# Kernel optimization log

Measured on AMD Instinct MI355X. Metric: run time of the kernel, lower is better.

The kernel has to match this reference:

```python
import jax, jax.numpy as jnp
import numpy as np
from jax import lax

# flat indices of the 8 'donut' taps in a 3x3 kernel (center position 4 stays zero),
# matching torch.nonzero row-major ordering of the mask
_DONUT_IDX = jnp.array([0, 1, 2, 3, 5, 6, 7, 8])

def _gelu(x):
    return jax.nn.gelu(x, approximate=False)  # torch nn.GELU default (erf)

def _conv(x, w, dil=1, pad=0):
    return lax.conv_general_dilated(x, w, (1, 1), [(pad, pad), (pad, pad)],
                                    rhs_dilation=(dil, dil),
                                    dimension_numbers=('NCHW', 'OIHW', 'NCHW'))

def _donut_conv(x, p, dil):
    # ParamConv_reg_variable_dilation with shuffle_true=0: scatter 8 params into a
    # 3x3 kernel (zero center) and conv with rhs_dilation=dil, padding=dil ('same').
    O, I, _ = p.shape
    k = jnp.zeros((O, I, 9), p.dtype).at[:, :, _DONUT_IDX].set(p).reshape(O, I, 3, 3)
    return _conv(x, k, dil=dil, pad=dil)

def _resblock(x, w1, w2):
    # gelu(Sequential(conv3x3, gelu, conv3x3)(x) + x)
    return _gelu(_conv(_gelu(_conv(x, w1, pad=1)), w2, pad=1) + x)

def _avgpool2(x):
    N, C, H, W = x.shape
    return x.reshape(N, C, H // 2, 2, W // 2, 2).mean(axis=(3, 5))

def _upsample(x, scale, w):
    # nn.Upsample(scale, bilinear, align_corners=False) -> half-pixel bilinear resize
    N, C, H, W = x.shape
    if scale > 1:
        x = jax.image.resize(x, (N, C, H * scale, W * scale), method='bilinear')
    return _gelu(_conv(x, w))  # 1x1 conv + gelu

def _shine_fwd(input_image, conv0a_w, conv0b_w, first_p, cl10_w, cl2_w,
               dil_p, dilres_p, ups_w, out1_w, out2_w, last_w):
    # n_frames=5, center frame index 2; H,W divisible by 64 so no pad branch
    target = input_image[:, 2:3]
    feats = jnp.concatenate([input_image[:, :2], input_image[:, 3:]], axis=1)  # [N,4,H,W]
    target = _gelu(_conv(target, conv0b_w))            # 1x1 -> 48 ch
    feats = _gelu(_conv(feats, conv0a_w, pad=1))       # 3x3 -> 16 ch
    base = jnp.concatenate([target, feats], axis=1)    # 64 ch

    outs = [_gelu(_donut_conv(base, first_p, 1))]      # first_output (dil 1)
    base = _resblock(base, cl10_w[0, 0], cl10_w[0, 1])
    outs.append(_gelu(_donut_conv(base, dilres_p[0], 3)))  # dilated_convs_res[0]
    base = _resblock(base, cl2_w[0, 0], cl2_w[0, 1])

    dils = (5, 8, 10, 11)     # dilated_convs effective dilations (add_dilation=0)
    dilres = (3, 6, 8, 9)     # dilated_convs_res effective dilations
    for i in range(4):
        m = _gelu(_donut_conv(base, dil_p[i], dils[i]))
        outs.append(_upsample(m, 2 ** i, ups_w[i]))
        if i < 3:
            base = _avgpool2(base)
            base = _resblock(base, cl10_w[i + 1, 0], cl10_w[i + 1, 1])
            m = _gelu(_donut_conv(base, dilres_p[i + 1], dilres[i + 1]))
            outs.append(_upsample(m, 2 ** (i + 1), ups_w[i + 1]))
            base = _resblock(base, cl2_w[i + 1, 0], cl2_w[i + 1, 1])

    out = jnp.concatenate(outs, axis=1)                # 9*64 = 576 ch
    out = _gelu(_conv(out, out1_w))                    # 1x1 576->288
    out = _gelu(_conv(out, out2_w))                    # 1x1 288->64
    return _conv(out, last_w)                          # 1x1 64->1

def setup_inputs():
    key = jax.random.key(0)
    ks = jax.random.split(key, 12)
    s = 0.05
    F = 64
    return {
        'input_image': jax.random.normal(ks[0], (2, 5, 256, 256), jnp.float32),
        'conv0a_w': jax.random.normal(ks[1], (16, 4, 3, 3), jnp.float32) * s,
        'conv0b_w': jax.random.normal(ks[2], (48, 1, 1, 1), jnp.float32) * s,
        'first_p': jax.random.normal(ks[3], (F, F, 8), jnp.float32) * s,
        'cl10_w': jax.random.normal(ks[4], (4, 2, F, F, 3, 3), jnp.float32) * s,
        'cl2_w': jax.random.normal(ks[5], (4, 2, F, F, 3, 3), jnp.float32) * s,
        'dil_p': jax.random.normal(ks[6], (4, F, F, 8), jnp.float32) * s,
        'dilres_p': jax.random.normal(ks[7], (4, F, F, 8), jnp.float32) * s,
        'ups_w': jax.random.normal(ks[8], (4, F, F, 1, 1), jnp.float32) * s,
        'out1_w': jax.random.normal(ks[9], (288, 576, 1, 1), jnp.float32) * s,
        'out2_w': jax.random.normal(ks[10], (64, 288, 1, 1), jnp.float32) * s,
        'last_w': jax.random.normal(ks[11], (1, 64, 1, 1), jnp.float32) * s,
    }

def reference(input_image, conv0a_w, conv0b_w, first_p, cl10_w, cl2_w,
              dil_p, dilres_p, ups_w, out1_w, out2_w, last_w):
    return _shine_fwd(input_image, conv0a_w, conv0b_w, first_p, cl10_w, cl2_w,
                      dil_p, dilres_p, ups_w, out1_w, out2_w, last_w)
```

## Files before the change

kernel.cpp:

```cpp
#include <hip/hip_runtime.h>
#include <hip/hip_bf16.h>


#define HPX 65536
#define FCH 64
#define CHPX 32768

typedef __attribute__((ext_vector_type(8))) short  short8;
typedef __attribute__((ext_vector_type(4))) float  floatx4;

__device__ __forceinline__ float gelu_f(float x) {
  return 0.5f * x * (1.0f + erff(x * 0.70710678118654752440f));
}
__device__ __forceinline__ unsigned short f2bf(float x) {
  unsigned u = __float_as_uint(x);
  unsigned r = (u + 0x7FFFu + ((u >> 16) & 1u)) >> 16;
  return (unsigned short)r;
}
__device__ __forceinline__ float bf2f(unsigned short h) {
  return __uint_as_float(((unsigned)h) << 16);
}

__global__ __launch_bounds__(256) void conv0_elem_kernel(
    const float* __restrict__ img,
    const float* __restrict__ w0b,
    unsigned short* __restrict__ ohi,
    unsigned short* __restrict__ olo)
{
  int t = blockIdx.x * 256 + threadIdx.x;
  int cg = t % 6;
  int pn = t / 6;
  int px = pn & (HPX - 1);
  int n  = pn >> 16;
  float x = img[(long)n * 5 * HPX + 2 * HPX + px];
  short8 oh, ol;
  #pragma unroll
  for (int j = 0; j < 8; j++) {
    int c = cg * 8 + j;
    float v = gelu_f(w0b[c] * x);
    unsigned short hb = f2bf(v);
    oh[j] = (short)hb;
    ol[j] = (short)f2bf(v - bf2f(hb));
  }
  long o = ((long)pn) * 64 + cg * 8;
  *(short8*)&ohi[o] = oh;
  *(short8*)&olo[o] = ol;
}

__global__ __launch_bounds__(256) void conv0_conv_kernel(
    const float* __restrict__ img,
    const float* __restrict__ w0a,
    unsigned short* __restrict__ ohi,
    unsigned short* __restrict__ olo)
{
  int t = blockIdx.x * 256 + threadIdx.x;
  int cg = t & 1;
  int pn = t >> 1;
  int px = pn & (HPX - 1);
  int n  = pn >> 16;
  int y = px >> 8, x = px & 255;
  const float* im = img + (long)n * 5 * HPX;
  const int map4[4] = {0, 1, 3, 4};
  float vreg[36];
  #pragma unroll
  for (int fi = 0; fi < 4; fi++)
    #pragma unroll
    for (int ky = 0; ky < 3; ky++)
      #pragma unroll
      for (int kx = 0; kx < 3; kx++) {
        int yy = y + ky - 1, xx = x + kx - 1;
        bool ok = ((unsigned)yy < 256u) && ((unsigned)xx < 256u);
        vreg[(fi * 3 + ky) * 3 + kx] =
            ok ? im[(long)map4[fi] * HPX + yy * 256 + xx] : 0.0f;
      }
  short8 oh, ol;
  #pragma unroll
  for (int j = 0; j < 8; j++) {
    int co = cg * 8 + j;
    const float* wr = w0a + co * 36;
    float r = 0.0f;
    #pragma unroll
    for (int q = 0; q < 36; q++) r = fmaf(wr[q], vreg[q], r);
    float v = gelu_f(r);
    unsigned short hb = f2bf(v);
    oh[j] = (short)hb;
    ol[j] = (short)f2bf(v - bf2f(hb));
  }
  long o = ((long)pn) * 64 + 48 + cg * 8;
  *(short8*)&ohi[o] = oh;
  *(short8*)&olo[o] = ol;
}

struct JobArr { int4 j[29]; };

__global__ __launch_bounds__(256) void pack_conv_kernel(
    const float* __restrict__ cl10, const float* __restrict__ cl2,
    const float* __restrict__ first_p, const float* __restrict__ dilres_p,
    const float* __restrict__ dil_p, const float* __restrict__ ups_w,
    unsigned short* __restrict__ packs, JobArr jobs)
{
  int4 jb = jobs.j[blockIdx.y];
  int ntaps = jb.z;
  int idx = blockIdx.x * 256 + threadIdx.x;
  if (idx >= ntaps * 8192) return;
  int j  = idx & 7;
  int l  = (idx >> 3) & 63;
  int s  = (idx >> 9) & 1;
  int nt = (idx >> 10) & 3;
  int kt = (idx >> 12) & 1;
  int tap = idx >> 13;
  int oc = nt * 16 + (l & 15);
  int ci = kt * 32 + (l >> 4) * 8 + j;
  const float* src;
  switch (jb.x) {
    case 0: src = cl10; break;
    case 1: src = cl2; break;
    case 2: src = first_p; break;
    case 3: src = dilres_p; break;
    case 4: src = dil_p; break;
    default: src = ups_w; break;
  }
  float w = src[jb.y + (oc * 64 + ci) * ntaps + tap];
  unsigned short hi = f2bf(w);
  unsigned short v = (s == 0) ? hi : f2bf(w - bf2f(hi));
  packs[jb.w + idx] = v;
}

__global__ __launch_bounds__(256) void pack_w1_kernel(
    const float* __restrict__ w1, unsigned short* __restrict__ w1p)
{
  int t = blockIdx.x * 256 + threadIdx.x;
  if (t >= 18 * 18 * 512) return;
  int j = t & 7, l = (t >> 3) & 63;
  int mt = (t >> 9) % 18, kt = (t >> 9) / 18;
  int oc = mt * 16 + (l & 15);
  int k  = kt * 32 + (l >> 4) * 8 + j;
  float w = w1[oc * 576 + k];
  unsigned short hi = f2bf(w);
  unsigned short lo = f2bf(w - bf2f(hi));
  long base = ((long)(kt * 18 + mt) * 2) * 512 + l * 8 + j;
  w1p[base] = hi;
  w1p[base + 512] = lo;
}
__global__ __launch_bounds__(256) void pack_w2_kernel(
    const float* __restrict__ w2, unsigned short* __restrict__ w2p)
{
  int t = blockIdx.x * 256 + threadIdx.x;
  if (t >= 9 * 4 * 512) return;
  int j = t & 7, l = (t >> 3) & 63;
  int ot = (t >> 9) % 4, kt = (t >> 9) / 4;
  int oc = ot * 16 + (l & 15);
  int k  = kt * 32 + (l >> 4) * 8 + j;
  float w = w2[oc * 288 + k];
  unsigned short hi = f2bf(w);
  unsigned short lo = f2bf(w - bf2f(hi));
  long base = ((long)(kt * 4 + ot) * 2) * 512 + l * 8 + j;
  w2p[base] = hi;
  w2p[base + 512] = lo;
}

template <int NTAPS, int MT, bool RESID, bool TO_CONCAT>
__global__ __launch_bounds__(256) void conv_pipe_kernel(
    const unsigned short* __restrict__ in_hi,
    const unsigned short* __restrict__ in_lo,
    const unsigned short* __restrict__ wp,
    const unsigned short* __restrict__ res_hi,
    const unsigned short* __restrict__ res_lo,
    unsigned short* __restrict__ out_hi,
    unsigned short* __restrict__ out_lo,
    int Hs, int logW, int dil, int ccol)
{
  __shared__ short8 wst[2][1024];
  __shared__ float  ftb[4][16][65];
  const int tid  = threadIdx.x;
  const int lane = tid & 63;
  const int wave = tid >> 6;
  const int row  = lane & 15;
  const int g    = lane >> 4;
  const int n    = blockIdx.z;
  const int Ws   = 1 << logW;
  const int npx_in = Hs << logW;
  const int opx0 = blockIdx.x * (64 * MT) + wave * (16 * MT);

  const unsigned short* ihi = in_hi + (long)n * npx_in * 64;
  const unsigned short* ilo = in_lo + (long)n * npx_in * 64;
  const short8* wpv = (const short8*)wp;

  int ry[MT], rx[MT];
  #pragma unroll
  for (int mt = 0; mt < MT; mt++) {
    int p = opx0 + mt * 16 + row;
    ry[mt] = p >> logW;
    rx[mt] = p & (Ws - 1);
  }

  floatx4 acc[MT][4];
  #pragma unroll
  for (int mt = 0; mt < MT; mt++)
    #pragma unroll
    for (int nt = 0; nt < 4; nt++) acc[mt][nt] = (floatx4){0.f, 0.f, 0.f, 0.f};

  const short8 zz = {0, 0, 0, 0, 0, 0, 0, 0};
  short8 sreg[4];
  short8 ahA[MT][2], alA[MT][2], ahB[MT][2], alB[MT][2];

  auto stage_issue = [&](int t) {
    #pragma unroll
    for (int p = 0; p < 4; p++)
      sreg[p] = wpv[(long)t * 1024 + tid + p * 256];
  };
  auto stage_write = [&](int b) {
    #pragma unroll
    for (int p = 0; p < 4; p++)
      wst[b][tid + p * 256] = sreg[p];
  };
  auto a_load = [&](short8 (&ah)[MT][2], short8 (&al)[MT][2], int t) {
    const int kk  = (NTAPS == 9) ? t : (t < 4 ? t : t + 1);
    const int dyd = (kk / 3 - 1) * dil, dxd = (kk % 3 - 1) * dil;
    #pragma unroll
    for (int mt = 0; mt < MT; mt++) {
      int yy = ry[mt] + dyd, xx = rx[mt] + dxd;
      bool ok = ((unsigned)yy < (unsigned)Hs) && ((unsigned)xx < (unsigned)Ws);
      long base = ok ? (long)((yy << logW) + xx) * 64 : 0;
      #pragma unroll
      for (int kt = 0; kt < 2; kt++) {
        long a = base + kt * 32 + g * 8;
        short8 h = *(const short8*)(ihi + a);
        short8 l = *(const short8*)(ilo + a);
        ah[mt][kt] = ok ? h : zz;
        al[mt][kt] = ok ? l : zz;
      }
    }
  };
  auto compute = [&](int b, short8 (&ah)[MT][2], short8 (&al)[MT][2]) {
    #pragma unroll
    for (int kt = 0; kt < 2; kt++)
      #pragma unroll
      for (int nt = 0; nt < 4; nt++) {
        short8 bh = wst[b][(kt * 4 + nt) * 128 + lane];
        short8 bl = wst[b][(kt * 4 + nt) * 128 + 64 + lane];
        #pragma unroll
        for (int mt = 0; mt < MT; mt++) {
          acc[mt][nt] = __builtin_amdgcn_mfma_f32_16x16x32_bf16(ah[mt][kt], bh, acc[mt][nt], 0, 0, 0);
          acc[mt][nt] = __builtin_amdgcn_mfma_f32_16x16x32_bf16(ah[mt][kt], bl, acc[mt][nt], 0, 0, 0);
          acc[mt][nt] = __builtin_amdgcn_mfma_f32_16x16x32_bf16(al[mt][kt], bh, acc[mt][nt], 0, 0, 0);
        }
      }
  };

  stage_issue(0);
  a_load(ahA, alA, 0);
  stage_write(0);
  __syncthreads();

  #pragma unroll
  for (int tt = 0; tt < NTAPS; tt++) {
    const int b = tt & 1;
    if (tt + 1 < NTAPS) {
      stage_issue(tt + 1);
      if ((tt & 1) == 0) a_load(ahB, alB, tt + 1);
      else               a_load(ahA, alA, tt + 1);
    }
    if ((tt & 1) == 0) compute(b, ahA, alA);
    else               compute(b, ahB, alB);
    if (tt + 1 < NTAPS) {
      stage_write(b ^ 1);
      __syncthreads();
    }
  }

  #pragma unroll
  for (int mt = 0; mt < MT; mt++) {
    __builtin_amdgcn_wave_barrier();
    #pragma unroll
    for (int nt = 0; nt < 4; nt++)
      #pragma unroll
      for (int r = 0; r < 4; r++)
        ftb[wave][g * 4 + r][nt * 16 + row] = acc[mt][nt][r];
    __builtin_amdgcn_wave_barrier();
    const int pxb = opx0 + mt * 16;
    const int pxl = lane >> 2;
    #pragma unroll
    for (int it = 0; it < 2; it++) {
      const int ch = (lane & 3) + it * 4;
      float vv[8];
      #pragma unroll
      for (int j = 0; j < 8; j++) vv[j] = ftb[wave][pxl][ch * 8 + j];
      if (RESID) {
        long rb = ((long)n * npx_in + pxb + pxl) * 64 + ch * 8;
        short8 rh = *(const short8*)(res_hi + rb);
        short8 rl = *(const short8*)(res_lo + rb);
        #pragma unroll
        for (int j = 0; j < 8; j++)
          vv[j] += bf2f((unsigned short)rh[j]) + bf2f((unsigned short)rl[j]);
      }
      short8 oh8, ol8;
      #pragma unroll
      for (int j = 0; j < 8; j++) {
        float v = gelu_f(vv[j]);
        unsigned short hb = f2bf(v);
        oh8[j] = (short)hb;
        ol8[j] = (short)f2bf(v - bf2f(hb));
      }
      if (TO_CONCAT) {
        *(short8*)&out_hi[((long)n * HPX + pxb + pxl) * 576 + ccol + ch * 8] = oh8;
      } else {
        *(short8*)&out_hi[((long)n * npx_in + pxb + pxl) * 64 + ch * 8] = oh8;
        *(short8*)&out_lo[((long)n * npx_in + pxb + pxl) * 64 + ch * 8] = ol8;
      }
    }
  }
}

template <int MT>
__global__ __launch_bounds__(256) void ups_mfma_kernel(
    const unsigned short* __restrict__ in_hi,
    const unsigned short* __restrict__ in_lo,
    const unsigned short* __restrict__ wp,
    unsigned short* __restrict__ outc,
    int Hs, int logW, int ccol)
{
  __shared__ short8 wst[1024];
  __shared__ unsigned short tb[4][16][76];
  const int tid  = threadIdx.x;
  const int lane = threadIdx.x & 63;
  const int wave = threadIdx.x >> 6;
  const int row  = lane & 15;
  const int g    = lane >> 4;
  const int n    = blockIdx.z;
  const int npx_in = Hs << logW;
  const int opx0 = blockIdx.x * (64 * MT) + wave * (16 * MT);

  const unsigned short* ihi = in_hi + (long)n * npx_in * 64;
  const unsigned short* ilo = in_lo + (long)n * npx_in * 64;
  const short8* wpv = (const short8*)wp;

  int b00[MT], b01[MT], b10[MT], b11[MT];
  float bwx[MT], bwy[MT];
  #pragma unroll
  for (int mt = 0; mt < MT; mt++) {
    int p = opx0 + mt * 16 + row;
    int Y = p >> 8, X = p & 255;
    float sc = (float)Hs * (1.0f / 256.0f);
    float fy = ((float)Y + 0.5f) * sc - 0.5f;
    float fx = ((float)X + 0.5f) * sc - 0.5f;
    int y0 = (int)floorf(fy), x0 = (int)floorf(fx);
    bwy[mt] = fy - (float)y0; bwx[mt] = fx - (float)x0;
    int y0c = min(max(y0, 0), Hs - 1), y1c = min(max(y0 + 1, 0), Hs - 1);
    int x0c = min(max(x0, 0), Hs - 1), x1c = min(max(x0 + 1, 0), Hs - 1);
    b00[mt] = (y0c * Hs + x0c) * 64; b01[mt] = (y0c * Hs + x1c) * 64;
    b10[mt] = (y1c * Hs + x0c) * 64; b11[mt] = (y1c * Hs + x1c) * 64;
  }

  floatx4 acc[MT][4];
  #pragma unroll
  for (int mt = 0; mt < MT; mt++)
    #pragma unroll
    for (int nt = 0; nt < 4; nt++) acc[mt][nt] = (floatx4){0.f, 0.f, 0.f, 0.f};

  #pragma unroll
  for (int p = 0; p < 4; p++)
    wst[tid + p * 256] = wpv[tid + p * 256];
  __syncthreads();

  #pragma unroll
  for (int kt = 0; kt < 2; kt++) {
    const int ko = kt * 32 + g * 8;
    short8 ah[MT], al[MT];
    #pragma unroll
    for (int mt = 0; mt < MT; mt++) {
      short8 h00 = *(const short8*)(ihi + b00[mt] + ko);
      short8 l00 = *(const short8*)(ilo + b00[mt] + ko);
      short8 h01 = *(const short8*)(ihi + b01[mt] + ko);
      short8 l01 = *(const short8*)(ilo + b01[mt] + ko);
      short8 h10 = *(const short8*)(ihi + b10[mt] + ko);
      short8 l10 = *(const short8*)(ilo + b10[mt] + ko);
      short8 h11 = *(const short8*)(ihi + b11[mt] + ko);
      short8 l11 = *(const short8*)(ilo + b11[mt] + ko);
      short8 hh, ll;
      #pragma unroll
      for (int j = 0; j < 8; j++) {
        float v00 = bf2f((unsigned short)h00[j]) + bf2f((unsigned short)l00[j]);
        float v01 = bf2f((unsigned short)h01[j]) + bf2f((unsigned short)l01[j]);
        float v10 = bf2f((unsigned short)h10[j]) + bf2f((unsigned short)l10[j]);
        float v11 = bf2f((unsigned short)h11[j]) + bf2f((unsigned short)l11[j]);
        float v0 = v00 + bwx[mt] * (v01 - v00);
        float v1 = v10 + bwx[mt] * (v11 - v10);
        float v  = v0 + bwy[mt] * (v1 - v0);
        unsigned short hb = f2bf(v);
        hh[j] = (short)hb;
        ll[j] = (short)f2bf(v - bf2f(hb));
      }
      ah[mt] = hh; al[mt] = ll;
    }
    #pragma unroll
    for (int nt = 0; nt < 4; nt++) {
      short8 bh = wst[(kt * 4 + nt) * 2 * 64 + lane];
      short8 bl = wst[((kt * 4 + nt) * 2 + 1) * 64 + lane];
      #pragma unroll
      for (int mt = 0; mt < MT; mt++) {
        acc[mt][nt] = __builtin_amdgcn_mfma_f32_16x16x32_bf16(ah[mt], bh, acc[mt][nt], 0, 0, 0);
        acc[mt][nt] = __builtin_amdgcn_mfma_f32_16x16x32_bf16(ah[mt], bl, acc[mt][nt], 0, 0, 0);
        acc[mt][nt] = __builtin_amdgcn_mfma_f32_16x16x32_bf16(al[mt], bh, acc[mt][nt], 0, 0, 0);
      }
    }
  }

  #pragma unroll
  for (int mt = 0; mt < MT; mt++) {
    __builtin_amdgcn_wave_barrier();
    #pragma unroll
    for (int nt = 0; nt < 4; nt++)
      #pragma unroll
      for (int r = 0; r < 4; r++)
        tb[wave][g * 4 + r][nt * 16 + row] = f2bf(gelu_f(acc[mt][nt][r]));
    __builtin_amdgcn_wave_barrier();
    const int pxb = opx0 + mt * 16;
    const int pxl = lane >> 2;
    #pragma unroll
    for (int it = 0; it < 2; it++) {
      int ch = (lane & 3) + it * 4;
      short8 v8 = *(const short8*)&tb[wave][pxl][ch * 8];
      *(short8*)&outc[((long)n * HPX + pxb + pxl) * 576 + ccol + ch * 8] = v8;
    }
  }
}

__global__ __launch_bounds__(256) void avgpool_nhwc_kernel(
    const unsigned short* __restrict__ ihi, const unsigned short* __restrict__ ilo,
    unsigned short* __restrict__ ohi, unsigned short* __restrict__ olo,
    int logWo)
{
  const int lognpo = 2 * logWo;
  long t = (long)blockIdx.x * 256 + threadIdx.x;
  int cg = (int)(t & 7);
  int p  = (int)((t >> 3) & ((1 << lognpo) - 1));
  int n  = (int)(t >> (3 + lognpo));
  int y = p >> logWo, x = p & ((1 << logWo) - 1);
  int Wi = 2 << logWo;
  long ib = ((long)n * (4 << lognpo) + (long)(2 * y) * Wi + 2 * x) * 64 + cg * 8;
  short8 h00 = *(const short8*)(ihi + ib);
  short8 h01 = *(const short8*)(ihi + ib + 64);
  short8 h10 = *(const short8*)(ihi + ib + (long)Wi * 64);
  short8 h11 = *(const short8*)(ihi + ib + (long)Wi * 64 + 64);
  short8 l00 = *(const short8*)(ilo + ib);
  short8 l01 = *(const short8*)(ilo + ib + 64);
  short8 l10 = *(const short8*)(ilo + ib + (long)Wi * 64);
  short8 l11 = *(const short8*)(ilo + ib + (long)Wi * 64 + 64);
  short8 oh, ol;
  #pragma unroll
  for (int j = 0; j < 8; j++) {
    float v = 0.25f * ((bf2f((unsigned short)h00[j]) + bf2f((unsigned short)l00[j])) +
                       (bf2f((unsigned short)h01[j]) + bf2f((unsigned short)l01[j])) +
                       (bf2f((unsigned short)h10[j]) + bf2f((unsigned short)l10[j])) +
                       (bf2f((unsigned short)h11[j]) + bf2f((unsigned short)l11[j])));
    unsigned short hb = f2bf(v);
    oh[j] = (short)hb;
    ol[j] = (short)f2bf(v - bf2f(hb));
  }
  long ob = (((long)n << lognpo) + p) * 64 + cg * 8;
  *(short8*)(ohi + ob) = oh;
  *(short8*)(olo + ob) = ol;
}

__global__ __launch_bounds__(256) void out1_gemm_kernel(
    const unsigned short* __restrict__ v,
    const unsigned short* __restrict__ w1p,
    unsigned short* __restrict__ h,
    int cpx)
{
  __shared__ short8 ws8[2400];
  const int tid  = threadIdx.x;
  const int lane = tid & 63;
  const int wave = tid >> 6;
  const int row  = lane & 15;
  const int g    = lane >> 4;
  const int n    = blockIdx.y;
  const int px0  = cpx + blockIdx.x * 64;
  const int mtb  = (wave < 2) ? wave * 5 : 10 + (wave - 2) * 4;
  const int MTN  = (wave < 2) ? 5 : 4;
  const short8* w1v = (const short8*)w1p;

  floatx4 acc[4][5];
  #pragma unroll
  for (int t = 0; t < 4; t++)
    #pragma unroll
    for (int m = 0; m < 5; m++) acc[t][m] = (floatx4){0.f, 0.f, 0.f, 0.f};

  for (int kt = 0; kt < 18; kt++) {
    __syncthreads();
    #pragma unroll
    for (int p = 0; p < 9; p++)
      ws8[tid + p * 256] = w1v[kt * 2304 + tid + p * 256];
    __syncthreads();

    short8 a[4];
    #pragma unroll
    for (int t = 0; t < 4; t++)
      a[t] = *(const short8*)(v + ((long)n * HPX + px0 + t * 16 + row) * 576 +
                              kt * 32 + g * 8);
    #pragma unroll
    for (int m = 0; m < 5; m++) {
      if (m < MTN) {
        short8 bh = ws8[((mtb + m) * 2 + 0) * 64 + lane];
        short8 bl = ws8[((mtb + m) * 2 + 1) * 64 + lane];
        #pragma unroll
        for (int t = 0; t < 4; t++) {
          acc[t][m] = __builtin_amdgcn_mfma_f32_16x16x32_bf16(a[t], bh, acc[t][m], 0, 0, 0);
          acc[t][m] = __builtin_amdgcn_mfma_f32_16x16x32_bf16(a[t], bl, acc[t][m], 0, 0, 0);
        }
      }
    }
  }

  __syncthreads();
  unsigned short* hs2 = (unsigned short*)ws8;
  #pragma unroll
  for (int m = 0; m < 5; m++) {
    if (m < MTN) {
      #pragma unroll
      for (int t = 0; t < 4; t++)
        #pragma unroll
        for (int r = 0; r < 4; r++)
          hs2[(t * 16 + g * 4 + r) * 300 + (mtb + m) * 16 + row] =
              f2bf(gelu_f(acc[t][m][r]));
    }
  }
  __syncthreads();
  #pragma unroll
  for (int p = 0; p < 9; p++) {
    int li = tid + p * 256;
    int px = li / 36, c16 = li % 36;
    short8 v8 = *(const short8*)&hs2[px * 300 + c16 * 8];
    *(short8*)&h[((long)n * CHPX + (px0 - cpx) + px) * 288 + c16 * 8] = v8;
  }
}

__global__ __launch_bounds__(256) void out2_gemm_kernel(
    const unsigned short* __restrict__ h,
    const unsigned short* __restrict__ w2p,
    const float* __restrict__ w3,
    float* __restrict__ out,
    int cpx)
{
  __shared__ short8 w2s[4608];
  const int tid  = threadIdx.x;
  const int lane = tid & 63;
  const int wave = tid >> 6;
  const int row  = lane & 15;
  const int g    = lane >> 4;
  const int n    = blockIdx.y;
  const int pxc  = blockIdx.x * 256 + wave * 64;
  const short8* w2v = (const short8*)w2p;

  #pragma unroll
  for (int p = 0; p < 18; p++)
    w2s[tid + p * 256] = w2v[tid + p * 256];
  __syncthreads();

  floatx4 acc2[4][4];
  #pragma unroll
  for (int t = 0; t < 4; t++)
    #pragma unroll
    for (int ot = 0; ot < 4; ot++) acc2[t][ot] = (floatx4){0.f, 0.f, 0.f, 0.f};

  for (int kt = 0; kt < 9; kt++) {
    short8 a[4];
    #pragma unroll
    for (int t = 0; t < 4; t++)
      a[t] = *(const short8*)&h[((long)n * CHPX + pxc + t * 16 + row) * 288 +
                                kt * 32 + g * 8];
    #pragma unroll
    for (int ot = 0; ot < 4; ot++) {
      short8 bh = w2s[((kt * 4 + ot) * 2 + 0) * 64 + lane];
      short8 bl = w2s[((kt * 4 + ot) * 2 + 1) * 64 + lane];
      #pragma unroll
      for (int t = 0; t < 4; t++) {
        acc2[t][ot] = __builtin_amdgcn_mfma_f32_16x16x32_bf16(a[t], bh, acc2[t][ot], 0, 0, 0);
        acc2[t][ot] = __builtin_amdgcn_mfma_f32_16x16x32_bf16(a[t], bl, acc2[t][ot], 0, 0, 0);
      }
    }
  }

  float w3r[4];
  #pragma unroll
  for (int ot = 0; ot < 4; ot++) w3r[ot] = w3[ot * 16 + row];
  #pragma unroll
  for (int t = 0; t < 4; t++) {
    float r[4] = {0.f, 0.f, 0.f, 0.f};
    #pragma unroll
    for (int ot = 0; ot < 4; ot++)
      #pragma unroll
      for (int rr = 0; rr < 4; rr++)
        r[rr] = fmaf(w3r[ot], gelu_f(acc2[t][ot][rr]), r[rr]);
    #pragma unroll
    for (int rr = 0; rr < 4; rr++) {
      r[rr] += __shfl_xor(r[rr], 1);
      r[rr] += __shfl_xor(r[rr], 2);
      r[rr] += __shfl_xor(r[rr], 4);
      r[rr] += __shfl_xor(r[rr], 8);
    }
    if (row == 0) {
      int px = cpx + pxc + t * 16 + g * 4;
      #pragma unroll
      for (int rr = 0; rr < 4; rr++)
        out[(long)n * HPX + px + rr] = r[rr];
    }
  }
}

extern "C" void kernel_launch(void* const* d_in, const int* in_sizes, int n_in,
                              void* d_out, int out_size, void* d_ws, size_t ws_size,
                              hipStream_t stream) {
  const float* img      = (const float*)d_in[0];
  const float* w0a      = (const float*)d_in[1];
  const float* w0b      = (const float*)d_in[2];
  const float* first_p  = (const float*)d_in[3];
  const float* cl10     = (const float*)d_in[4];
  const float* cl2      = (const float*)d_in[5];
  const float* dil_p    = (const float*)d_in[6];
  const float* dilres_p = (const float*)d_in[7];
  const float* ups_w    = (const float*)d_in[8];
  const float* w1       = (const float*)d_in[9];
  const float* w2       = (const float*)d_in[10];
  const float* w3       = (const float*)d_in[11];

  const size_t CONCAT_B = 150994944ul;
  const size_t ACT_B    = 16777216ul;
  const size_t PACKS_B  = 3604480ul;
  const size_t W1P_B    = 663552ul;
  const size_t W2P_B    = 73728ul;
  const size_t NEED = CONCAT_B + 4 * ACT_B + PACKS_B + W1P_B + W2P_B;

  if (ws_size < NEED) {
    hipMemsetAsync(d_out, 0, (size_t)out_size * 4, stream);
    return;
  }

  char* wsb = (char*)d_ws;
  unsigned short* concat = (unsigned short*)wsb;
  unsigned short* Xhi = (unsigned short*)(wsb + CONCAT_B);
  unsigned short* Xlo = (unsigned short*)(wsb + CONCAT_B + ACT_B);
  unsigned short* Yhi = (unsigned short*)(wsb + CONCAT_B + 2 * ACT_B);
  unsigned short* Ylo = (unsigned short*)(wsb + CONCAT_B + 3 * ACT_B);
  unsigned short* packs = (unsigned short*)(wsb + CONCAT_B + 4 * ACT_B);
  unsigned short* w1p = (unsigned short*)(wsb + CONCAT_B + 4 * ACT_B + PACKS_B);
  unsigned short* w2p = (unsigned short*)(wsb + CONCAT_B + 4 * ACT_B + PACKS_B + W1P_B);
  unsigned short* hbuf = Xhi;

  auto off_cl10   = [](int c) { return (long)c * 73728; };
  auto off_cl2    = [](int c) { return 589824l + (long)c * 73728; };
  const long OFF_FIRST = 1179648;
  auto off_dilres = [](int k) { return 1245184l + (long)k * 65536; };
  auto off_dil    = [](int k) { return 1507328l + (long)k * 65536; };
  auto off_ups    = [](int k) { return 1769472l + (long)k * 8192; };

  JobArr jobs;
  for (int c = 0; c < 8; c++) jobs.j[c]     = {0, c * 36864, 9, (int)off_cl10(c)};
  for (int c = 0; c < 8; c++) jobs.j[8 + c] = {1, c * 36864, 9, (int)off_cl2(c)};
  jobs.j[16] = {2, 0, 8, (int)OFF_FIRST};
  for (int k = 0; k < 4; k++) jobs.j[17 + k] = {3, k * 32768, 8, (int)off_dilres(k)};
  for (int k = 0; k < 4; k++) jobs.j[21 + k] = {4, k * 32768, 8, (int)off_dil(k)};
  for (int k = 0; k < 4; k++) jobs.j[25 + k] = {5, k * 4096, 1, (int)off_ups(k)};
  pack_conv_kernel<<<dim3(288, 29), 256, 0, stream>>>(
      cl10, cl2, first_p, dilres_p, dil_p, ups_w, packs, jobs);
  pack_w1_kernel<<<(18 * 18 * 512 + 255) / 256, 256, 0, stream>>>(w1, w1p);
  pack_w2_kernel<<<(9 * 4 * 512 + 255) / 256, 256, 0, stream>>>(w2, w2p);

  conv0_elem_kernel<<<(2 * HPX * 6) / 256, 256, 0, stream>>>(img, w0b, Xhi, Xlo);
  conv0_conv_kernel<<<(2 * HPX * 2) / 256, 256, 0, stream>>>(img, w0a, Xhi, Xlo);

  auto conv9 = [&](const unsigned short* ih, const unsigned short* il, long wo,
                   unsigned short* oh, unsigned short* ol, int Hs, int logW) {
    int npx = Hs << logW;
    if (npx == HPX)
      conv_pipe_kernel<9, 2, false, false><<<dim3(npx / 128, 1, 2), 256, 0, stream>>>(
          ih, il, packs + wo, nullptr, nullptr, oh, ol, Hs, logW, 1, 0);
    else
      conv_pipe_kernel<9, 1, false, false><<<dim3(npx / 64, 1, 2), 256, 0, stream>>>(
          ih, il, packs + wo, nullptr, nullptr, oh, ol, Hs, logW, 1, 0);
  };
  auto conv9r = [&](const unsigned short* ih, const unsigned short* il, long wo,
                    unsigned short* rh, unsigned short* rl, int Hs, int logW) {
    int npx = Hs << logW;
    if (npx == HPX)
      conv_pipe_kernel<9, 2, true, false><<<dim3(npx / 128, 1, 2), 256, 0, stream>>>(
          ih, il, packs + wo, rh, rl, rh, rl, Hs, logW, 1, 0);
    else
      conv_pipe_kernel<9, 1, true, false><<<dim3(npx / 64, 1, 2), 256, 0, stream>>>(
          ih, il, packs + wo, rh, rl, rh, rl, Hs, logW, 1, 0);
  };
  auto donutC = [&](const unsigned short* ih, const unsigned short* il, long wo,
                    int dil, int ccol) {
    conv_pipe_kernel<8, 2, false, true><<<dim3(512, 1, 2), 256, 0, stream>>>(
        ih, il, packs + wo, nullptr, nullptr, concat, nullptr, 256, 8, dil, ccol);
  };
  auto donutA = [&](const unsigned short* ih, const unsigned short* il, long wo,
                    int dil, unsigned short* oh, unsigned short* ol, int Hs, int logW) {
    int npx = Hs << logW;
    if (npx == HPX)
      conv_pipe_kernel<8, 2, false, false><<<dim3(npx / 128, 1, 2), 256, 0, stream>>>(
          ih, il, packs + wo, nullptr, nullptr, oh, ol, Hs, logW, dil, 0);
    else
      conv_pipe_kernel<8, 1, false, false><<<dim3(npx / 64, 1, 2), 256, 0, stream>>>(
          ih, il, packs + wo, nullptr, nullptr, oh, ol, Hs, logW, dil, 0);
  };
  auto upsC = [&](const unsigned short* ih, const unsigned short* il, long wo,
                  int Hs, int logW, int ccol) {
    ups_mfma_kernel<4><<<dim3(256, 1, 2), 256, 0, stream>>>(
        ih, il, packs + wo, concat, Hs, logW, ccol);
  };
  auto avgp = [&](const unsigned short* ih, const unsigned short* il,
                  unsigned short* oh, unsigned short* ol, int logWo) {
    long total = 2l * (1l << (2 * logWo)) * 8;
    avgpool_nhwc_kernel<<<(int)(total / 256), 256, 0, stream>>>(ih, il, oh, ol, logWo);
  };

  donutC(Xhi, Xlo, OFF_FIRST, 1, 0);
  conv9(Xhi, Xlo, off_cl10(0), Yhi, Ylo, 256, 8);
  conv9r(Yhi, Ylo, off_cl10(1), Xhi, Xlo, 256, 8);
  donutC(Xhi, Xlo, off_dilres(0), 3, 64);
  conv9(Xhi, Xlo, off_cl2(0), Yhi, Ylo, 256, 8);
  conv9r(Yhi, Ylo, off_cl2(1), Xhi, Xlo, 256, 8);

  donutA(Xhi, Xlo, off_dil(0), 5, Yhi, Ylo, 256, 8);
  upsC(Yhi, Ylo, off_ups(0), 256, 8, 128);
  avgp(Xhi, Xlo, Yhi, Ylo, 7);
  conv9(Yhi, Ylo, off_cl10(2), Xhi, Xlo, 128, 7);
  conv9r(Xhi, Xlo, off_cl10(3), Yhi, Ylo, 128, 7);
  donutA(Yhi, Ylo, off_dilres(1), 6, Xhi, Xlo, 128, 7);
  upsC(Xhi, Xlo, off_ups(1), 128, 7, 192);
  conv9(Yhi, Ylo, off_cl2(2), Xhi, Xlo, 128, 7);
  conv9r(Xhi, Xlo, off_cl2(3), Yhi, Ylo, 128, 7);

  donutA(Yhi, Ylo, off_dil(1), 8, Xhi, Xlo, 128, 7);
  upsC(Xhi, Xlo, off_ups(1), 128, 7, 256);
  avgp(Yhi, Ylo, Xhi, Xlo, 6);
  conv9(Xhi, Xlo, off_cl10(4), Yhi, Ylo, 64, 6);
  conv9r(Yhi, Ylo, off_cl10(5), Xhi, Xlo, 64, 6);
  donutA(Xhi, Xlo, off_dilres(2), 8, Yhi, Ylo, 64, 6);
  upsC(Yhi, Ylo, off_ups(2), 64, 6, 320);
  conv9(Xhi, Xlo, off_cl2(4), Yhi, Ylo, 64, 6);
  conv9r(Yhi, Ylo, off_cl2(5), Xhi, Xlo, 64, 6);

  donutA(Xhi, Xlo, off_dil(2), 10, Yhi, Ylo, 64, 6);
  upsC(Yhi, Ylo, off_ups(2), 64, 6, 384);
  avgp(Xhi, Xlo, Yhi, Ylo, 5);
  conv9(Yhi, Ylo, off_cl10(6), Xhi, Xlo, 32, 5);
  conv9r(Xhi, Xlo, off_cl10(7), Yhi, Ylo, 32, 5);
  donutA(Yhi, Ylo, off_dilres(3), 9, Xhi, Xlo, 32, 5);
  upsC(Xhi, Xlo, off_ups(3), 32, 5, 448);
  conv9(Yhi, Ylo, off_cl2(6), Xhi, Xlo, 32, 5);
  conv9r(Xhi, Xlo, off_cl2(7), Yhi, Ylo, 32, 5);

  donutA(Yhi, Ylo, off_dil(3), 11, Xhi, Xlo, 32, 5);
  upsC(Xhi, Xlo, off_ups(3), 32, 5, 512);

  for (int c = 0; c < 2; c++) {
    out1_gemm_kernel<<<dim3(CHPX / 64, 2), 256, 0, stream>>>(
        concat, w1p, hbuf, c * CHPX);
    out2_gemm_kernel<<<dim3(CHPX / 256, 2), 256, 0, stream>>>(
        hbuf, w2p, w3, (float*)d_out, c * CHPX);
  }
}
```

Measured before the change: 972.3 us.

## Double-buffer out1 GEMM weights and retile waves to cover all output channels

The out1 GEMM kernel now double-buffers the weight tiles in shared memory, prefetching the next k-tile into registers while the current one feeds MFMA, so each k-step needs one barrier instead of two. The work split also changes: each block handles 128 pixels and each wave owns 32 pixels across all 18 output channel tiles, instead of splitting channel tiles across waves over 64 pixels. The aim is to amortize weight staging over more pixels and hide global load latency. In exchange each wave holds 36 accumulators, which raises register pressure and may reduce occupancy, and the grid has half as many blocks.

```diff
diff --git a/kernel.cpp b/kernel.cpp
--- a/kernel.cpp
+++ b/kernel.cpp
@@ -469,69 +469,92 @@
     unsigned short* __restrict__ h,
     int cpx)
 {
-  __shared__ short8 ws8[2400];
+  __shared__ short8 wst[2][2304];
   const int tid  = threadIdx.x;
   const int lane = tid & 63;
   const int wave = tid >> 6;
   const int row  = lane & 15;
   const int g    = lane >> 4;
   const int n    = blockIdx.y;
-  const int px0  = cpx + blockIdx.x * 64;
-  const int mtb  = (wave < 2) ? wave * 5 : 10 + (wave - 2) * 4;
-  const int MTN  = (wave < 2) ? 5 : 4;
+  const int px0  = cpx + blockIdx.x * 128;
+  const int wpx  = px0 + wave * 32;
   const short8* w1v = (const short8*)w1p;
-
-  floatx4 acc[4][5];
-  #pragma unroll
-  for (int t = 0; t < 4; t++)
-    #pragma unroll
-    for (int m = 0; m < 5; m++) acc[t][m] = (floatx4){0.f, 0.f, 0.f, 0.f};
-
+  const unsigned short* vn = v + ((long)n * HPX + wpx) * 576;
+
+  floatx4 acc[2][18];
+  #pragma unroll
+  for (int t = 0; t < 2; t++)
+    #pragma unroll
+    for (int mt = 0; mt < 18; mt++) acc[t][mt] = (floatx4){0.f, 0.f, 0.f, 0.f};
+
+  short8 sreg[9];
+  short8 aA[2], aB[2];
+
+  auto stage_issue = [&](int kt) {
+    #pragma unroll
+    for (int p = 0; p < 9; p++)
+      sreg[p] = w1v[kt * 2304 + tid + p * 256];
+  };
+  auto stage_write = [&](int b) {
+    #pragma unroll
+    for (int p = 0; p < 9; p++)
+      wst[b][tid + p * 256] = sreg[p];
+  };
+  auto a_load = [&](short8 (&a)[2], int kt) {
+    #pragma unroll
+    for (int t = 0; t < 2; t++)
+      a[t] = *(const short8*)(vn + (long)(t * 16 + row) * 576 + kt * 32 + g * 8);
+  };
+  auto compute = [&](int b, short8 (&a)[2]) {
+    #pragma unroll
+    for (int mt = 0; mt < 18; mt++) {
+      short8 bh = wst[b][(mt * 2 + 0) * 64 + lane];
+      short8 bl = wst[b][(mt * 2 + 1) * 64 + lane];
+      #pragma unroll
+      for (int t = 0; t < 2; t++) {
+        acc[t][mt] = __builtin_amdgcn_mfma_f32_16x16x32_bf16(a[t], bh, acc[t][mt], 0, 0, 0);
+        acc[t][mt] = __builtin_amdgcn_mfma_f32_16x16x32_bf16(a[t], bl, acc[t][mt], 0, 0, 0);
+      }
+    }
+  };
+
+  stage_issue(0);
+  a_load(aA, 0);
+  stage_write(0);
+  __syncthreads();
+
+  #pragma unroll 2
   for (int kt = 0; kt < 18; kt++) {
-    __syncthreads();
-    #pragma unroll
-    for (int p = 0; p < 9; p++)
-      ws8[tid + p * 256] = w1v[kt * 2304 + tid + p * 256];
-    __syncthreads();
-
-    short8 a[4];
-    #pragma unroll
-    for (int t = 0; t < 4; t++)
-      a[t] = *(const short8*)(v + ((long)n * HPX + px0 + t * 16 + row) * 576 +
-                              kt * 32 + g * 8);
-    #pragma unroll
-    for (int m = 0; m < 5; m++) {
-      if (m < MTN) {
-        short8 bh = ws8[((mtb + m) * 2 + 0) * 64 + lane];
-        short8 bl = ws8[((mtb + m) * 2 + 1) * 64 + lane];
-        #pragma unroll
-        for (int t = 0; t < 4; t++) {
-          acc[t][m] = __builtin_amdgcn_mfma_f32_16x16x32_bf16(a[t], bh, acc[t][m], 0, 0, 0);
-          acc[t][m] = __builtin_amdgcn_mfma_f32_16x16x32_bf16(a[t], bl, acc[t][m], 0, 0, 0);
-        }
-      }
+    const int b = kt & 1;
+    if (kt + 1 < 18) {
+      stage_issue(kt + 1);
+      if ((kt & 1) == 0) a_load(aB, kt + 1);
+      else               a_load(aA, kt + 1);
+    }
+    if ((kt & 1) == 0) compute(b, aA);
+    else               compute(b, aB);
+    if (kt + 1 < 18) {
+      stage_write(b ^ 1);
+      __syncthreads();
     }
   }
 
   __syncthreads();
-  unsigned short* hs2 = (unsigned short*)ws8;
-  #pragma unroll
-  for (int m = 0; m < 5; m++) {
-    if (m < MTN) {
-      #pragma unroll
-      for (int t = 0; t < 4; t++)
-        #pragma unroll
-        for (int r = 0; r < 4; r++)
-          hs2[(t * 16 + g * 4 + r) * 300 + (mtb + m) * 16 + row] =
-              f2bf(gelu_f(acc[t][m][r]));
-    }
-  }
+  unsigned short* hs2 = (unsigned short*)wst;
+  #pragma unroll
+  for (int t = 0; t < 2; t++)
+    #pragma unroll
+    for (int mt = 0; mt < 18; mt++)
+      #pragma unroll
+      for (int r = 0; r < 4; r++)
+        hs2[(wave * 32 + t * 16 + g * 4 + r) * 288 + mt * 16 + row] =
+            f2bf(gelu_f(acc[t][mt][r]));
   __syncthreads();
   #pragma unroll
-  for (int p = 0; p < 9; p++) {
+  for (int p = 0; p < 18; p++) {
     int li = tid + p * 256;
     int px = li / 36, c16 = li % 36;
-    short8 v8 = *(const short8*)&hs2[px * 300 + c16 * 8];
+    short8 v8 = *(const short8*)&hs2[px * 288 + c16 * 8];
     *(short8*)&h[((long)n * CHPX + (px0 - cpx) + px) * 288 + c16 * 8] = v8;
   }
 }
@@ -757,7 +780,7 @@
   upsC(Xhi, Xlo, off_ups(3), 32, 5, 512);
 
   for (int c = 0; c < 2; c++) {
-    out1_gemm_kernel<<<dim3(CHPX / 64, 2), 256, 0, stream>>>(
+    out1_gemm_kernel<<<dim3(CHPX / 128, 2), 256, 0, stream>>>(
         concat, w1p, hbuf, c * CHPX);
     out2_gemm_kernel<<<dim3(CHPX / 256, 2), 256, 0, stream>>>(
         hbuf, w2p, w3, (float*)d_out, c * CHPX);
```

Measured after the change: 1.001 ms. 1.03x slower.
